# Performance work log

Measured on AMD Instinct MI355X. Metric: run time of the kernel, lower is better.

## Reference

```python
import jax, jax.numpy as jnp
import numpy as np

DIM = 1024
HEADS = 16


def setup_inputs() -> dict:
    key = jax.random.key(0)
    ks = jax.random.split(key, 9)
    B, N, C = 2, 2048, DIM
    hd = C // HEADS
    s = 1.0 / np.sqrt(C)
    x = jax.random.normal(ks[0], (B, N, C), dtype=jnp.float32)
    wq = jax.random.normal(ks[1], (C, C), dtype=jnp.float32) * s
    wk = jax.random.normal(ks[2], (C, C), dtype=jnp.float32) * s
    wv = jax.random.normal(ks[3], (C, C), dtype=jnp.float32) * s
    wp = jax.random.normal(ks[4], (C, C), dtype=jnp.float32) * s
    bp = jnp.zeros((C,), dtype=jnp.float32)
    # rotary table: angles theta_j = 10000^{-2j/hd}, positions 0..N-1
    inv_freq = 1.0 / (10000.0 ** (jnp.arange(0, hd, 2, dtype=jnp.float32) / hd))
    ang = jnp.arange(N, dtype=jnp.float32)[:, None] * inv_freq[None, :]  # (N, hd//2)
    cos = jnp.cos(ang)
    sin = jnp.sin(ang)
    return {"x": x, "wq": wq, "wk": wk, "wv": wv, "wp": wp, "bp": bp,
            "cos": cos, "sin": sin, "num_heads": HEADS}


def _apply_rotary(t, cos, sin):
    # t: (B, N, H, D); cos/sin: (N, D//2) -> broadcast (1, N, 1, D//2)
    B, N, H, D = t.shape
    tr = t.reshape(B, N, H, D // 2, 2)
    t1, t2 = tr[..., 0], tr[..., 1]
    c = cos[None, :, None, :]
    s = sin[None, :, None, :]
    o1 = t1 * c - t2 * s
    o2 = t1 * s + t2 * c
    return jnp.stack([o1, o2], axis=-1).reshape(B, N, H, D)


def reference(x, wq, wk, wv, wp, bp, cos, sin, num_heads):
    B, N, C = x.shape
    H = num_heads
    D = C // H
    q = (x @ wq.T).reshape(B, N, H, D)
    k = (x @ wk.T).reshape(B, N, H, D)
    v = (x @ wv.T).reshape(B, N, H, D)
    q = _apply_rotary(q, cos, sin)
    k = _apply_rotary(k, cos, sin)
    scale = 1.0 / jnp.sqrt(jnp.asarray(D, dtype=x.dtype))
    # scores: (B, H, N, N)
    scores = jnp.einsum('bnhd,bmhd->bhnm', q, k) * scale
    attn = jax.nn.softmax(scores, axis=-1)
    out = jnp.einsum('bhnm,bmhd->bnhd', attn, v).reshape(B, N, C)
    return out @ wp.T + bp
```

## Files before the change

### kernel.cpp

```cpp
#include <hip/hip_runtime.h>
#include <hip/hip_bf16.h>
#include <stdint.h>

#define DEVI __device__ __forceinline__

using bf16 = __hip_bfloat16;
typedef __bf16 bf16x8 __attribute__((ext_vector_type(8)));
typedef float f32x4 __attribute__((ext_vector_type(4)));

static constexpr int Bb = 2, Nn = 2048, Cc = 1024, Hh = 16, Dd = 64;
static constexpr float CSC = 0.125f * 1.44269504088896340736f;

DEVI bf16 f2bf(float x) {
  __bf16 h = (__bf16)x;
  return *(bf16*)&h;
}
DEVI float fexp2(float x) { return __builtin_amdgcn_exp2f(x); }

DEVI bf16x8 cvt8(f32x4 a, f32x4 b) {
  bf16x8 r;
  r[0] = (__bf16)a[0]; r[1] = (__bf16)a[1]; r[2] = (__bf16)a[2]; r[3] = (__bf16)a[3];
  r[4] = (__bf16)b[0]; r[5] = (__bf16)b[1]; r[6] = (__bf16)b[2]; r[7] = (__bf16)b[3];
  return r;
}

DEVI void gld_lds16(const bf16* g, bf16* l) {
  __builtin_amdgcn_global_load_lds(
      (__attribute__((address_space(1))) void*)(g),
      (__attribute__((address_space(3))) void*)(l),
      16, 0, 0);
}

__global__ __launch_bounds__(256) void k_cvt(const float* __restrict__ x,
                                             const float* __restrict__ wq,
                                             const float* __restrict__ wk,
                                             const float* __restrict__ wv,
                                             const float* __restrict__ wp,
                                             bf16* xb, bf16* wqb, bf16* wkb,
                                             bf16* wvb, bf16* wpb) {
  int bid = blockIdx.x;
  const float* src; bf16* dst; size_t off;
  if (bid < 2048) {
    src = x; dst = xb; off = (size_t)bid * 2048;
  } else {
    int s = (bid - 2048) >> 9, r = (bid - 2048) & 511;
    off = (size_t)r * 2048;
    src = s == 0 ? wq : s == 1 ? wk : s == 2 ? wv : wp;
    dst = s == 0 ? wqb : s == 1 ? wkb : s == 2 ? wvb : wpb;
  }
  size_t i = off + (size_t)threadIdx.x * 8;
  f32x4 a = *(const f32x4*)(src + i);
  f32x4 b = *(const f32x4*)(src + i + 4);
  *(bf16x8*)(dst + i) = cvt8(a, b);
}

template <int MFC, class Epi>
DEVI void gemm_lds_body(const bf16* __restrict__ A, const bf16* __restrict__ Bw,
                        int K, int m0, int n0, bf16* lA, bf16* lB, Epi epi) {
  constexpr int BM = MFC * 32;
  constexpr int PA = BM / 64;
  const int t = threadIdx.x;
  const int lane = t & 63, wave = t >> 6;
  const int wr = wave >> 1, wc = wave & 1;

  f32x4 acc[MFC][4] = {};

  for (int k0 = 0; k0 < K; k0 += 32) {
    __syncthreads();
#pragma unroll
    for (int p = 0; p < PA; ++p) {
      int c = p * 256 + t;
      int row = c >> 2, col = (c & 3) * 8;
      gld_lds16(A + (size_t)(m0 + row) * K + k0 + col,
                lA + (size_t)(p * 256 + wave * 64) * 8);
    }
#pragma unroll
    for (int p = 0; p < 2; ++p) {
      int c = p * 256 + t;
      int row = c >> 2, col = (c & 3) * 8;
      gld_lds16(Bw + (size_t)(n0 + row) * K + k0 + col,
                lB + (size_t)(p * 256 + wave * 64) * 8);
    }
    __syncthreads();

    bf16x8 aF[MFC];
#pragma unroll
    for (int mf = 0; mf < MFC; ++mf)
      aF[mf] = *(const bf16x8*)(lA + (wr * (BM / 2) + mf * 16 + (lane & 15)) * 32 + (lane >> 4) * 8);
#pragma unroll
    for (int nf = 0; nf < 4; ++nf) {
      bf16x8 bF = *(const bf16x8*)(lB + (wc * 64 + nf * 16 + (lane & 15)) * 32 + (lane >> 4) * 8);
#pragma unroll
      for (int mf = 0; mf < MFC; ++mf)
        acc[mf][nf] = __builtin_amdgcn_mfma_f32_16x16x32_bf16(aF[mf], bF, acc[mf][nf], 0, 0, 0);
    }
  }

#pragma unroll
  for (int mf = 0; mf < MFC; ++mf)
#pragma unroll
    for (int nf = 0; nf < 4; ++nf)
#pragma unroll
      for (int r = 0; r < 4; ++r) {
        int gm = m0 + wr * (BM / 2) + mf * 16 + (lane >> 4) * 4 + r;
        int gn = n0 + wc * 64 + nf * 16 + (lane & 15);
        epi(gm, gn, acc[mf][nf][r]);
      }
}

struct EpiRope {
  bf16* dst; const float* cosw; const float* sinw; float scale;
  DEVI void operator()(int gm, int gn, float v) const {
    int b = gm >> 11, n = gm & 2047;
    int h = gn >> 6, d = gn & 63;
    int i = d >> 1;
    float c = cosw[n * 32 + i], s = sinw[n * 32 + i];
    float p = __shfl_xor(v, 1);
    float o = (d & 1) ? (p * s + v * c) : (v * c - p * s);
    dst[((size_t)(b * Hh + h) * Nn + n) * 64 + d] = f2bf(o * scale);
  }
};

struct EpiVt {
  bf16* dst;
  DEVI void operator()(int gm, int gn, float v) const {
    int h = gm >> 6, d = gm & 63;
    int b = gn >> 11, n = gn & 2047;
    dst[((size_t)(b * Hh + h) * 64 + d) * Nn + n] = f2bf(v);
  }
};

struct EpiProj {
  float* dst; const float* bias;
  DEVI void operator()(int gm, int gn, float v) const {
    dst[(size_t)gm * Cc + gn] = v + bias[gn];
  }
};

__global__ __launch_bounds__(256) void k_qkv(const bf16* __restrict__ xb,
                                             const bf16* __restrict__ wqb,
                                             const bf16* __restrict__ wkb,
                                             const bf16* __restrict__ wvb,
                                             bf16* q_ws, bf16* k_ws, bf16* vt_ws,
                                             const float* __restrict__ cw,
                                             const float* __restrict__ sw) {
  __shared__ __align__(16) bf16 smem[256 * 32];
  bf16* lA = smem;
  bf16* lB = smem + 128 * 32;
  int bid = blockIdx.x;
  if (bid < 512) {
    int sub = bid & 255;
    int m0 = (sub >> 3) * 128, n0 = (sub & 7) * 128;
    bool isq = bid < 256;
    gemm_lds_body<4>(xb, isq ? wqb : wkb, Cc, m0, n0, lA, lB,
                     EpiRope{isq ? q_ws : k_ws, cw, sw, isq ? CSC : 1.0f});
  } else {
    int sub = bid - 512;
    int m0 = (sub & 7) * 128, n0 = (sub >> 3) * 128;
    gemm_lds_body<4>(wvb, xb, Cc, m0, n0, lA, lB, EpiVt{vt_ws});
  }
}

__global__ __launch_bounds__(256) void k_proj(const bf16* __restrict__ A,
                                              const bf16* __restrict__ W,
                                              float* dst, const float* __restrict__ bias) {
  __shared__ __align__(16) bf16 smem[192 * 32];
  gemm_lds_body<2>(A, W, Cc, blockIdx.x * 64, blockIdx.y * 128,
                   smem, smem + 64 * 32, EpiProj{dst, bias});
}

__global__ __launch_bounds__(256) void k_flash(const bf16* __restrict__ q_ws,
                                               const bf16* __restrict__ k_ws,
                                               const bf16* __restrict__ vt_ws,
                                               bf16* __restrict__ attn_o) {
  __shared__ __align__(16) bf16 lK[2][64 * 64];
  __shared__ __align__(16) bf16 lV[2][64 * 64];
  __shared__ __align__(16) bf16 pbuf[4][16 * 64];

  const int t = threadIdx.x, lane = t & 63, wave = t >> 6;
  const int bh = blockIdx.y;
  const int q0 = blockIdx.x * 64 + wave * 16;
  const bf16* qg = q_ws + (size_t)bh * Nn * 64;
  const bf16* kg = k_ws + (size_t)bh * Nn * 64;
  const bf16* vg = vt_ws + (size_t)bh * 64 * Nn;

  bf16x8 qF[2];
#pragma unroll
  for (int kd = 0; kd < 2; ++kd)
    qF[kd] = *(const bf16x8*)(qg + (size_t)(q0 + (lane & 15)) * 64 + kd * 32 + (lane >> 4) * 8);

  f32x4 accO[4] = {};
  float LsL[4] = {0.f, 0.f, 0.f, 0.f};

  bf16x8 rk[2], rv[2];
  auto load_tile = [&](int kt) {
#pragma unroll
    for (int p = 0; p < 2; ++p) {
      int c = p * 256 + t;
      int row = c >> 3, col = (c & 7) * 8;
      rk[p] = *(const bf16x8*)(kg + (size_t)(kt * 64 + row) * 64 + col);
      rv[p] = *(const bf16x8*)(vg + (size_t)row * Nn + kt * 64 + col);
    }
  };
  auto store_tile = [&](int buf) {
#pragma unroll
    for (int p = 0; p < 2; ++p) {
      int c = p * 256 + t;
      int row = c >> 3;
      int idx = (row * 64 + (c & 7) * 8) ^ ((row & 7) << 3);
      *(bf16x8*)(lK[buf] + idx) = rk[p];
      *(bf16x8*)(lV[buf] + idx) = rv[p];
    }
  };

  load_tile(0);
  store_tile(0);
  __syncthreads();

  constexpr int NT = Nn / 64;
  for (int kt = 0; kt < NT; ++kt) {
    const int cur = kt & 1;
    if (kt + 1 < NT) load_tile(kt + 1);

    f32x4 accS[4];
#pragma unroll
    for (int nf = 0; nf < 4; ++nf) {
      int row = nf * 16 + (lane & 15);
      int i0 = (row * 64 + 0 * 32 + (lane >> 4) * 8) ^ ((row & 7) << 3);
      int i1 = (row * 64 + 1 * 32 + (lane >> 4) * 8) ^ ((row & 7) << 3);
      bf16x8 kF0 = *(const bf16x8*)(lK[cur] + i0);
      bf16x8 kF1 = *(const bf16x8*)(lK[cur] + i1);
      f32x4 sacc = {};
      sacc = __builtin_amdgcn_mfma_f32_16x16x32_bf16(qF[0], kF0, sacc, 0, 0, 0);
      sacc = __builtin_amdgcn_mfma_f32_16x16x32_bf16(qF[1], kF1, sacc, 0, 0, 0);
      accS[nf] = sacc;
    }

#pragma unroll
    for (int nf = 0; nf < 4; ++nf)
#pragma unroll
      for (int r = 0; r < 4; ++r) {
        float pv = fexp2(accS[nf][r]);
        LsL[r] += pv;
        int prow = (lane >> 4) * 4 + r;
        int pidx = (prow * 64 + nf * 16 + (lane & 15)) ^ ((prow & 7) << 3);
        pbuf[wave][pidx] = f2bf(pv);
      }

#pragma unroll
    for (int kd = 0; kd < 2; ++kd) {
      int prow = lane & 15;
      int pidx = (prow * 64 + kd * 32 + (lane >> 4) * 8) ^ ((prow & 7) << 3);
      bf16x8 pF = *(const bf16x8*)(&pbuf[wave][pidx]);
#pragma unroll
      for (int nf = 0; nf < 4; ++nf) {
        int row = nf * 16 + (lane & 15);
        int iv = (row * 64 + kd * 32 + (lane >> 4) * 8) ^ ((row & 7) << 3);
        bf16x8 vF = *(const bf16x8*)(lV[cur] + iv);
        accO[nf] = __builtin_amdgcn_mfma_f32_16x16x32_bf16(pF, vF, accO[nf], 0, 0, 0);
      }
    }

    if (kt + 1 < NT) store_tile(cur ^ 1);
    __syncthreads();
  }

  float Ls[4];
#pragma unroll
  for (int r = 0; r < 4; ++r) {
    float s = LsL[r];
    s += __shfl_xor(s, 1);
    s += __shfl_xor(s, 2);
    s += __shfl_xor(s, 4);
    s += __shfl_xor(s, 8);
    Ls[r] = s;
  }

  const int b = bh >> 4, h = bh & 15;
#pragma unroll
  for (int r = 0; r < 4; ++r) {
    float inv = 1.0f / Ls[r];
    int qrow = q0 + (lane >> 4) * 4 + r;
#pragma unroll
    for (int nf = 0; nf < 4; ++nf) {
      int d = nf * 16 + (lane & 15);
      attn_o[((size_t)(b * Nn + qrow)) * Cc + h * 64 + d] = f2bf(accO[nf][r] * inv);
    }
  }
}

extern "C" void kernel_launch(void* const* d_in, const int* in_sizes, int n_in,
                              void* d_out, int out_size, void* d_ws, size_t ws_size,
                              hipStream_t stream) {
  (void)in_sizes; (void)n_in; (void)out_size; (void)ws_size;
  const float* x  = (const float*)d_in[0];
  const float* wq = (const float*)d_in[1];
  const float* wk = (const float*)d_in[2];
  const float* wv = (const float*)d_in[3];
  const float* wp = (const float*)d_in[4];
  const float* bp = (const float*)d_in[5];
  const float* cw = (const float*)d_in[6];
  const float* sw = (const float*)d_in[7];
  float* out = (float*)d_out;

  const size_t M1 = 1u << 20;
  bf16* x_bf  = (bf16*)d_ws;
  bf16* wq_bf = x_bf + 4 * M1;
  bf16* wk_bf = wq_bf + M1;
  bf16* wv_bf = wk_bf + M1;
  bf16* wp_bf = wv_bf + M1;
  bf16* q_ws  = wp_bf + M1;
  bf16* k_ws  = q_ws + 4 * M1;
  bf16* vt_ws = k_ws + 4 * M1;
  bf16* ao_ws = x_bf;

  k_cvt  <<<dim3(4096),    dim3(256), 0, stream>>>(x, wq, wk, wv, wp,
                                                   x_bf, wq_bf, wk_bf, wv_bf, wp_bf);
  k_qkv  <<<dim3(768),     dim3(256), 0, stream>>>(x_bf, wq_bf, wk_bf, wv_bf,
                                                   q_ws, k_ws, vt_ws, cw, sw);
  k_flash<<<dim3(32, 32),  dim3(256), 0, stream>>>(q_ws, k_ws, vt_ws, ao_ws);
  k_proj <<<dim3(64, 8),   dim3(256), 0, stream>>>(ao_ws, wp_bf, out, bp);
}
```

Before: 135.3 us.

## Process two 16-row query sub-tiles per wave in flash attention

```diff
diff --git a/kernel.cpp b/kernel.cpp
--- a/kernel.cpp
+++ b/kernel.cpp
@@ -175,22 +175,24 @@
                                                bf16* __restrict__ attn_o) {
   __shared__ __align__(16) bf16 lK[2][64 * 64];
   __shared__ __align__(16) bf16 lV[2][64 * 64];
-  __shared__ __align__(16) bf16 pbuf[4][16 * 64];
+  __shared__ __align__(16) bf16 pbuf[4][32 * 64];
 
   const int t = threadIdx.x, lane = t & 63, wave = t >> 6;
   const int bh = blockIdx.y;
-  const int q0 = blockIdx.x * 64 + wave * 16;
+  const int q0 = blockIdx.x * 128 + wave * 32;
   const bf16* qg = q_ws + (size_t)bh * Nn * 64;
   const bf16* kg = k_ws + (size_t)bh * Nn * 64;
   const bf16* vg = vt_ws + (size_t)bh * 64 * Nn;
 
-  bf16x8 qF[2];
-#pragma unroll
-  for (int kd = 0; kd < 2; ++kd)
-    qF[kd] = *(const bf16x8*)(qg + (size_t)(q0 + (lane & 15)) * 64 + kd * 32 + (lane >> 4) * 8);
-
-  f32x4 accO[4] = {};
-  float LsL[4] = {0.f, 0.f, 0.f, 0.f};
+  bf16x8 qF[2][2];
+#pragma unroll
+  for (int qs = 0; qs < 2; ++qs)
+#pragma unroll
+    for (int kd = 0; kd < 2; ++kd)
+      qF[qs][kd] = *(const bf16x8*)(qg + (size_t)(q0 + qs * 16 + (lane & 15)) * 64 + kd * 32 + (lane >> 4) * 8);
+
+  f32x4 accO[2][4] = {};
+  float LsL[2][4] = {};
 
   bf16x8 rk[2], rv[2];
   auto load_tile = [&](int kt) {
@@ -222,7 +224,7 @@
     const int cur = kt & 1;
     if (kt + 1 < NT) load_tile(kt + 1);
 
-    f32x4 accS[4];
+    f32x4 accS[2][4];
 #pragma unroll
     for (int nf = 0; nf < 4; ++nf) {
       int row = nf * 16 + (lane & 15);
@@ -230,34 +232,45 @@
       int i1 = (row * 64 + 1 * 32 + (lane >> 4) * 8) ^ ((row & 7) << 3);
       bf16x8 kF0 = *(const bf16x8*)(lK[cur] + i0);
       bf16x8 kF1 = *(const bf16x8*)(lK[cur] + i1);
-      f32x4 sacc = {};
-      sacc = __builtin_amdgcn_mfma_f32_16x16x32_bf16(qF[0], kF0, sacc, 0, 0, 0);
-      sacc = __builtin_amdgcn_mfma_f32_16x16x32_bf16(qF[1], kF1, sacc, 0, 0, 0);
-      accS[nf] = sacc;
-    }
-
-#pragma unroll
-    for (int nf = 0; nf < 4; ++nf)
-#pragma unroll
-      for (int r = 0; r < 4; ++r) {
-        float pv = fexp2(accS[nf][r]);
-        LsL[r] += pv;
-        int prow = (lane >> 4) * 4 + r;
-        int pidx = (prow * 64 + nf * 16 + (lane & 15)) ^ ((prow & 7) << 3);
-        pbuf[wave][pidx] = f2bf(pv);
-      }
+#pragma unroll
+      for (int qs = 0; qs < 2; ++qs) {
+        f32x4 sacc = {};
+        sacc = __builtin_amdgcn_mfma_f32_16x16x32_bf16(qF[qs][0], kF0, sacc, 0, 0, 0);
+        sacc = __builtin_amdgcn_mfma_f32_16x16x32_bf16(qF[qs][1], kF1, sacc, 0, 0, 0);
+        accS[qs][nf] = sacc;
+      }
+    }
+
+#pragma unroll
+    for (int qs = 0; qs < 2; ++qs)
+#pragma unroll
+      for (int nf = 0; nf < 4; ++nf)
+#pragma unroll
+        for (int r = 0; r < 4; ++r) {
+          float pv = fexp2(accS[qs][nf][r]);
+          LsL[qs][r] += pv;
+          int prow = qs * 16 + (lane >> 4) * 4 + r;
+          int pidx = (prow * 64 + nf * 16 + (lane & 15)) ^ ((prow & 7) << 3);
+          pbuf[wave][pidx] = f2bf(pv);
+        }
 
 #pragma unroll
     for (int kd = 0; kd < 2; ++kd) {
-      int prow = lane & 15;
-      int pidx = (prow * 64 + kd * 32 + (lane >> 4) * 8) ^ ((prow & 7) << 3);
-      bf16x8 pF = *(const bf16x8*)(&pbuf[wave][pidx]);
+      bf16x8 pF[2];
+#pragma unroll
+      for (int qs = 0; qs < 2; ++qs) {
+        int prow = qs * 16 + (lane & 15);
+        int pidx = (prow * 64 + kd * 32 + (lane >> 4) * 8) ^ ((prow & 7) << 3);
+        pF[qs] = *(const bf16x8*)(&pbuf[wave][pidx]);
+      }
 #pragma unroll
       for (int nf = 0; nf < 4; ++nf) {
         int row = nf * 16 + (lane & 15);
         int iv = (row * 64 + kd * 32 + (lane >> 4) * 8) ^ ((row & 7) << 3);
         bf16x8 vF = *(const bf16x8*)(lV[cur] + iv);
-        accO[nf] = __builtin_amdgcn_mfma_f32_16x16x32_bf16(pF, vF, accO[nf], 0, 0, 0);
+#pragma unroll
+        for (int qs = 0; qs < 2; ++qs)
+          accO[qs][nf] = __builtin_amdgcn_mfma_f32_16x16x32_bf16(pF[qs], vF, accO[qs][nf], 0, 0, 0);
       }
     }
 
@@ -265,28 +278,24 @@
     __syncthreads();
   }
 
-  float Ls[4];
-#pragma unroll
-  for (int r = 0; r < 4; ++r) {
-    float s = LsL[r];
-    s += __shfl_xor(s, 1);
-    s += __shfl_xor(s, 2);
-    s += __shfl_xor(s, 4);
-    s += __shfl_xor(s, 8);
-    Ls[r] = s;
-  }
-
   const int b = bh >> 4, h = bh & 15;
 #pragma unroll
-  for (int r = 0; r < 4; ++r) {
-    float inv = 1.0f / Ls[r];
-    int qrow = q0 + (lane >> 4) * 4 + r;
-#pragma unroll
-    for (int nf = 0; nf < 4; ++nf) {
-      int d = nf * 16 + (lane & 15);
-      attn_o[((size_t)(b * Nn + qrow)) * Cc + h * 64 + d] = f2bf(accO[nf][r] * inv);
-    }
-  }
+  for (int qs = 0; qs < 2; ++qs)
+#pragma unroll
+    for (int r = 0; r < 4; ++r) {
+      float s = LsL[qs][r];
+      s += __shfl_xor(s, 1);
+      s += __shfl_xor(s, 2);
+      s += __shfl_xor(s, 4);
+      s += __shfl_xor(s, 8);
+      float inv = 1.0f / s;
+      int qrow = q0 + qs * 16 + (lane >> 4) * 4 + r;
+#pragma unroll
+      for (int nf = 0; nf < 4; ++nf) {
+        int d = nf * 16 + (lane & 15);
+        attn_o[((size_t)(b * Nn + qrow)) * Cc + h * 64 + d] = f2bf(accO[qs][nf][r] * inv);
+      }
+    }
 }
 
 extern "C" void kernel_launch(void* const* d_in, const int* in_sizes, int n_in,
@@ -318,6 +327,6 @@
                                                    x_bf, wq_bf, wk_bf, wv_bf, wp_bf);
   k_qkv  <<<dim3(768),     dim3(256), 0, stream>>>(x_bf, wq_bf, wk_bf, wv_bf,
                                                    q_ws, k_ws, vt_ws, cw, sw);
-  k_flash<<<dim3(32, 32),  dim3(256), 0, stream>>>(q_ws, k_ws, vt_ws, ao_ws);
+  k_flash<<<dim3(16, 32),  dim3(256), 0, stream>>>(q_ws, k_ws, vt_ws, ao_ws);
   k_proj <<<dim3(64, 8),   dim3(256), 0, stream>>>(ao_ws, wp_bf, out, bp);
 }
```

Result: faster. 131.1 us (-3.1%).
